# Optimization experiments

Hardware: AMD Instinct MI355X
Metric: run time of the kernel (lower is better)

The kernel has to match this reference:

```python
import jax, jax.numpy as jnp
import numpy as np

N_KNN = 20
BN_EPS = 1e-5
LRELU_SLOPE = 0.2


def setup_inputs() -> dict:
    key = jax.random.key(0)
    k1, k2, k3 = jax.random.split(key, 3)
    B, C, N = 4, 3, 8192
    x = jax.random.normal(k1, (B, C, N), dtype=jnp.float32)
    # Conv2d(1, 16, 1): weight [16,1,1,1] -> flatten to [16]; bias [16]
    conv_w = jax.random.normal(k2, (16,), dtype=jnp.float32) * (1.0 / np.sqrt(1.0))
    conv_b = jax.random.normal(k3, (16,), dtype=jnp.float32) * 0.01
    gamma = jnp.ones((16,), dtype=jnp.float32)
    beta = jnp.zeros((16,), dtype=jnp.float32)
    return {"x": x, "conv_w": conv_w, "conv_b": conv_b, "gamma": gamma, "beta": beta}


def reference(x, conv_w, conv_b, gamma, beta):
    # x: [B, C, N]
    pts = jnp.transpose(x, (0, 2, 1))  # [B, N, C]
    sq = jnp.sum(pts * pts, axis=-1)  # [B, N]
    # pairwise squared distances, clamped for numerical safety
    d2 = sq[:, :, None] + sq[:, None, :] - 2.0 * jnp.einsum("bnc,bmc->bnm", pts, pts)
    d2 = jnp.maximum(d2, 0.0)
    # safe sqrt: zero gradient at zero distance (matches torch.cdist behavior)
    dist = jnp.where(d2 > 0, jnp.sqrt(jnp.where(d2 > 0, d2, 1.0)), 0.0)  # [B, N, N]
    # k smallest distances = k largest of negated
    neg_topk, _ = jax.lax.top_k(-dist, N_KNN)
    knn = -neg_topk  # [B, N, K], ascending
    # 1x1 conv (1 -> 16 channels): feat[b,c,n,k] = w[c]*knn[b,n,k] + b[c]
    feat = knn[:, None, :, :] * conv_w[None, :, None, None] + conv_b[None, :, None, None]  # [B,16,N,K]
    # BatchNorm2d in training mode: per-channel stats over (B, N, K), biased variance
    mean = jnp.mean(feat, axis=(0, 2, 3), keepdims=True)
    var = jnp.mean((feat - mean) ** 2, axis=(0, 2, 3), keepdims=True)
    xhat = (feat - mean) * jax.lax.rsqrt(var + BN_EPS)
    y = gamma[None, :, None, None] * xhat + beta[None, :, None, None]
    # LeakyReLU(0.2)
    y = jnp.where(y >= 0, y, LRELU_SLOPE * y)
    # max over k neighbors
    return jnp.max(y, axis=-1)  # [B, 16, N]
```

## Files before the change

kernel.cpp:

```cpp
#include <hip/hip_runtime.h>
#include <stdint.h>

#define NPTS  8192
#define NB    4
#define KNN   20
#define NROWS (NB * NPTS)
#define MTOTF 655360.0f
#define WPB   8
#define BLK   (WPB * 64)
#define SLICE (NPTS / WPB)
#define LSTR  (KNN + 1)
#define CAP   12
#define NEG_INF -3.0e38f

__device__ __forceinline__ float med3f(float a, float b, float c) {
    return __builtin_amdgcn_fmed3f(a, b, c);
}

__device__ __forceinline__ unsigned enc_f(float f) {
    unsigned u = __float_as_uint(f);
    return (u & 0x80000000u) ? ~u : (u | 0x80000000u);
}
__device__ __forceinline__ float dec_f(unsigned u) {
    return __uint_as_float((u & 0x80000000u) ? (u & 0x7fffffffu) : ~u);
}

__device__ __forceinline__ void insert_t(float arr[KNN], float t) {
#pragma unroll
    for (int j = KNN - 1; j > 0; --j) arr[j] = med3f(t, arr[j - 1], arr[j]);
    arr[0] = fmaxf(arr[0], t);
}

__device__ __forceinline__ void flush_buf(float arr[KNN], int& cnt,
    const float* bufw, int lane, unsigned* threshS) {
#pragma unroll
    for (int s = 0; s < CAP; ++s) {
        const float v = bufw[s * 64 + lane];
        insert_t(arr, (s < cnt) ? v : NEG_INF);
    }
    cnt = 0;
    atomicMax(&threshS[lane], enc_f(arr[KNN - 1]));
}

__device__ __forceinline__ void finalize_row(
    float arr[KNN], float px, float py, float pz, int row, int lane,
    float* __restrict__ kmaxA, float* __restrict__ kminA, float* __restrict__ acc)
{
    const float pn2 = px * px + py * py + pz * pz;
    float sum = 0.f, sum2 = 0.f, dmin = 0.f, dmax = 0.f;
#pragma unroll
    for (int k = 0; k < KNN; ++k) {
        float d2 = fmaxf(fmaf(-2.f, arr[k], pn2), 0.f);
        float d = sqrtf(d2);
        sum += d; sum2 += d2;
        if (k == 0) dmin = d;
        dmax = d;
    }
    kmaxA[row] = dmax;
    kminA[row] = dmin;
#pragma unroll
    for (int o = 32; o; o >>= 1) {
        sum  += __shfl_down(sum,  o, 64);
        sum2 += __shfl_down(sum2, o, 64);
    }
    if (lane == 0) { atomicAdd(acc, sum); atomicAdd(acc + 1, sum2); }
}

__global__ __launch_bounds__(256) void prep_kernel(
    const float* __restrict__ x, float4* __restrict__ tile4, float* __restrict__ acc)
{
    const int i = blockIdx.x * 256 + threadIdx.x;
    const int b = i >> 13;
    const int m = i & (NPTS - 1);
    const float* xb = x + b * 3 * NPTS;
    const float qx = xb[m], qy = xb[NPTS + m], qz = xb[2 * NPTS + m];
    tile4[i] = make_float4(qx, qy, qz, -0.5f * (qx * qx + qy * qy + qz * qz));
    if (i < 2) acc[i] = 0.f;
}

__global__ __launch_bounds__(BLK, 8) void knn_kernel(
    const float* __restrict__ x, const float4* __restrict__ tile4,
    float* __restrict__ kmaxA, float* __restrict__ kminA, float* __restrict__ acc)
{
    __shared__ float shmem[(WPB - 1) * 64 * LSTR];
    __shared__ unsigned threshS[64];

    const int tid  = threadIdx.x;
    const int lane = tid & 63;
    const int wave = __builtin_amdgcn_readfirstlane(tid >> 6);
    const int rowBase = blockIdx.x * 64;
    const int row  = rowBase + lane;
    const int b    = rowBase >> 13;
    const int n    = row & (NPTS - 1);
    const float* xb = x + b * 3 * NPTS;

    const float px = xb[n];
    const float py = xb[NPTS + n];
    const float pz = xb[2 * NPTS + n];

    if (tid < 64) threshS[tid] = enc_f(NEG_INF);

    float arr[KNN];
#pragma unroll
    for (int j = 0; j < KNN; ++j) arr[j] = NEG_INF;

    float* bufw = shmem + wave * (CAP * 64);
    int cnt = 0;
    __syncthreads();

    const float4* __restrict__ tp = tile4 + b * NPTS + wave * SLICE;
    float th = NEG_INF;
    for (int c = 0; c < SLICE / 32; ++c) {
        th = dec_f(*(volatile unsigned*)(threshS + lane));
        const float4* tq = tp + c * 32;
        for (int g = 0; g < 8; ++g) {
#pragma unroll
            for (int u = 0; u < 4; ++u) {
                const float4 q = tq[g * 4 + u];
                const float t = fmaf(q.x, px, fmaf(q.y, py, fmaf(q.z, pz, q.w)));
                if (t > th) { bufw[cnt * 64 + lane] = t; ++cnt; }
            }
            if (__any(cnt > CAP - 4)) {
                flush_buf(arr, cnt, bufw, lane, threshS);
                th = dec_f(*(volatile unsigned*)(threshS + lane));
            }
        }
    }
    if (__any(cnt > 0)) flush_buf(arr, cnt, bufw, lane, threshS);
    __syncthreads();

    if (wave > 0) {
        float* dst = shmem + ((wave - 1) * 64 + lane) * LSTR;
#pragma unroll
        for (int j = 0; j < KNN; ++j) dst[j] = arr[j];
    }
    __syncthreads();

    if (wave == 0) {
        for (int wsrc = 0; wsrc < WPB - 1; ++wsrc) {
            const float* src = shmem + (wsrc * 64 + lane) * LSTR;
#pragma unroll
            for (int k = 0; k < KNN; ++k) insert_t(arr, src[k]);
        }
        finalize_row(arr, px, py, pz, row, lane, kmaxA, kminA, acc);
    }
}

__global__ __launch_bounds__(BLK) void knn_kernel_lds(
    const float* __restrict__ x,
    float* __restrict__ kmaxA, float* __restrict__ kminA, float* __restrict__ acc)
{
    __shared__ float4 tile[2048];
    __shared__ float  lists[(WPB - 1) * 64 * LSTR];

    const int tid  = threadIdx.x;
    const int lane = tid & 63;
    const int wave = tid >> 6;
    const int rowBase = blockIdx.x * 64;
    const int row  = rowBase + lane;
    const int b    = rowBase >> 13;
    const int n    = row & (NPTS - 1);
    const float* xb = x + b * 3 * NPTS;

    const float px = xb[n];
    const float py = xb[NPTS + n];
    const float pz = xb[2 * NPTS + n];

    float arr[KNN];
#pragma unroll
    for (int j = 0; j < KNN; ++j) arr[j] = NEG_INF;

    for (int t0 = 0; t0 < NPTS; t0 += 2048) {
        __syncthreads();
        const int i4 = tid * 4;
        const float4 qx4 = *(const float4*)(xb + t0 + i4);
        const float4 qy4 = *(const float4*)(xb + NPTS + t0 + i4);
        const float4 qz4 = *(const float4*)(xb + 2 * NPTS + t0 + i4);
        tile[i4 + 0] = make_float4(qx4.x, qy4.x, qz4.x, -0.5f * (qx4.x*qx4.x + qy4.x*qy4.x + qz4.x*qz4.x));
        tile[i4 + 1] = make_float4(qx4.y, qy4.y, qz4.y, -0.5f * (qx4.y*qx4.y + qy4.y*qy4.y + qz4.y*qz4.y));
        tile[i4 + 2] = make_float4(qx4.z, qy4.z, qz4.z, -0.5f * (qx4.z*qx4.z + qy4.z*qy4.z + qz4.z*qz4.z));
        tile[i4 + 3] = make_float4(qx4.w, qy4.w, qz4.w, -0.5f * (qx4.w*qx4.w + qy4.w*qy4.w + qz4.w*qz4.w));
        __syncthreads();
        const float4* base = tile + wave * 256;
#pragma unroll 4
        for (int i = 0; i < 256; ++i) {
            const float4 q = base[i];
            float t = fmaf(q.x, px, fmaf(q.y, py, fmaf(q.z, pz, q.w)));
            insert_t(arr, t);
        }
    }
    __syncthreads();

    if (wave > 0) {
        float* dst = lists + ((wave - 1) * 64 + lane) * LSTR;
#pragma unroll
        for (int j = 0; j < KNN; ++j) dst[j] = arr[j];
    }
    __syncthreads();

    if (wave == 0) {
        for (int wsrc = 0; wsrc < WPB - 1; ++wsrc) {
            const float* src = lists + (wsrc * 64 + lane) * LSTR;
#pragma unroll
            for (int k = 0; k < KNN; ++k) insert_t(arr, src[k]);
        }
        finalize_row(arr, px, py, pz, row, lane, kmaxA, kminA, acc);
    }
}

__global__ __launch_bounds__(256) void out_kernel(
    const float* __restrict__ kmaxA, const float* __restrict__ kminA,
    const float* __restrict__ acc,
    const float* __restrict__ w, const float* __restrict__ gamma,
    const float* __restrict__ beta, float* __restrict__ out)
{
    const int r = blockIdx.x * 256 + threadIdx.x;
    const int b = r >> 13;
    const int n = r & (NPTS - 1);
    const float mu  = acc[0] * (1.0f / MTOTF);
    float var = acc[1] * (1.0f / MTOTF) - mu * mu;
    var = fmaxf(var, 0.f);
    const float kmax = kmaxA[r];
    const float kmin = kminA[r];
#pragma unroll
    for (int c = 0; c < 16; ++c) {
        const float wc = w[c];
        const float a = gamma[c] * wc * rsqrtf(wc * wc * var + 1e-5f);
        const float d = beta[c] - a * mu;
        float v = a * (a >= 0.f ? kmax : kmin) + d;
        v = (v >= 0.f) ? v : 0.2f * v;
        out[(b * 16 + c) * NPTS + n] = v;
    }
}

extern "C" void kernel_launch(void* const* d_in, const int* in_sizes, int n_in,
                              void* d_out, int out_size, void* d_ws, size_t ws_size,
                              hipStream_t stream)
{
    const float* x     = (const float*)d_in[0];
    const float* w     = (const float*)d_in[1];
    const float* gamma = (const float*)d_in[3];
    const float* beta  = (const float*)d_in[4];
    float* out = (float*)d_out;
    float* ws  = (float*)d_ws;

    float* kmaxA = ws;
    float* kminA = ws + NROWS;
    float* acc   = ws + 2 * NROWS;
    float4* tile4 = (float4*)(ws + 2 * NROWS + 4);
    const size_t need = (size_t)(2 * NROWS + 4) * 4 + (size_t)NROWS * 16;

    if (ws_size >= need) {
        prep_kernel<<<NROWS / 256, 256, 0, stream>>>(x, tile4, acc);
        knn_kernel<<<NROWS / 64, BLK, 0, stream>>>(x, tile4, kmaxA, kminA, acc);
    } else {
        prep_kernel<<<1, 256, 0, stream>>>(x, tile4, acc);
        knn_kernel_lds<<<NROWS / 64, BLK, 0, stream>>>(x, kmaxA, kminA, acc);
    }
    out_kernel<<<NROWS / 256, 256, 0, stream>>>(kmaxA, kminA, acc, w, gamma, beta, out);
}
```

Measured before the change: 206.3 us.

## Split KNN candidate scan into two halves per row block and merge

The candidate scan now runs as two blocks per 64-row group, each covering half of the points, and writes partial top-20 lists to workspace. A new merge kernel combines the two lists and finalizes the statistics. The buffered flush is also made dynamic with a larger buffer that skips empty groups of four. The aim is more blocks in flight to fill the GPU, at the cost of an extra kernel launch, extra global traffic for the partial lists, and weaker pruning thresholds within each half.

```diff
diff --git a/kernel.cpp b/kernel.cpp
--- a/kernel.cpp
+++ b/kernel.cpp
@@ -9,8 +9,11 @@
 #define WPB   8
 #define BLK   (WPB * 64)
 #define SLICE (NPTS / WPB)
+#define HALF  (NPTS / 2)
+#define SLICE2 (HALF / WPB)
 #define LSTR  (KNN + 1)
 #define CAP   12
+#define CAP2  16
 #define NEG_INF -3.0e38f
 
 __device__ __forceinline__ float med3f(float a, float b, float c) {
@@ -37,6 +40,22 @@
     for (int s = 0; s < CAP; ++s) {
         const float v = bufw[s * 64 + lane];
         insert_t(arr, (s < cnt) ? v : NEG_INF);
+    }
+    cnt = 0;
+    atomicMax(&threshS[lane], enc_f(arr[KNN - 1]));
+}
+
+__device__ __forceinline__ void flush_dyn(float arr[KNN], int& cnt,
+    const float* bufw, int lane, unsigned* threshS) {
+#pragma unroll
+    for (int s0 = 0; s0 < CAP2; s0 += 4) {
+        if (__any(cnt > s0)) {
+#pragma unroll
+            for (int s = s0; s < s0 + 4; ++s) {
+                const float v = bufw[s * 64 + lane];
+                insert_t(arr, (s < cnt) ? v : NEG_INF);
+            }
+        }
     }
     cnt = 0;
     atomicMax(&threshS[lane], enc_f(arr[KNN - 1]));
@@ -76,6 +95,115 @@
     const float qx = xb[m], qy = xb[NPTS + m], qz = xb[2 * NPTS + m];
     tile4[i] = make_float4(qx, qy, qz, -0.5f * (qx * qx + qy * qy + qz * qz));
     if (i < 2) acc[i] = 0.f;
+}
+
+__global__ __launch_bounds__(BLK, 8) void knn_split_kernel(
+    const float* __restrict__ x, const float4* __restrict__ tile4,
+    float* __restrict__ part)
+{
+    __shared__ float shmem[(WPB - 1) * 64 * LSTR];
+    __shared__ unsigned threshS[64];
+
+    const int tid  = threadIdx.x;
+    const int lane = tid & 63;
+    const int wave = __builtin_amdgcn_readfirstlane(tid >> 6);
+    const int rb   = blockIdx.x >> 1;
+    const int half = blockIdx.x & 1;
+    const int rowBase = rb * 64;
+    const int row  = rowBase + lane;
+    const int b    = rowBase >> 13;
+    const int n    = row & (NPTS - 1);
+    const float* xb = x + b * 3 * NPTS;
+
+    const float px = xb[n];
+    const float py = xb[NPTS + n];
+    const float pz = xb[2 * NPTS + n];
+
+    if (tid < 64) threshS[tid] = enc_f(NEG_INF);
+
+    float arr[KNN];
+#pragma unroll
+    for (int j = 0; j < KNN; ++j) arr[j] = NEG_INF;
+
+    float* bufw = shmem + wave * (CAP2 * 64);
+    __syncthreads();
+
+    const float4* __restrict__ tp = tile4 + b * NPTS + half * HALF + wave * SLICE2;
+
+#pragma unroll 8
+    for (int i = 0; i < 32; ++i) {
+        const float4 q = tp[i];
+        insert_t(arr, fmaf(q.x, px, fmaf(q.y, py, fmaf(q.z, pz, q.w))));
+    }
+    atomicMax(&threshS[lane], enc_f(arr[KNN - 1]));
+
+    int cnt = 0;
+    for (int c = 1; c < SLICE2 / 32; ++c) {
+        float th = dec_f(*(volatile unsigned*)(threshS + lane));
+        const float4* tq = tp + c * 32;
+        for (int g = 0; g < 8; ++g) {
+#pragma unroll
+            for (int u = 0; u < 4; ++u) {
+                const float4 q = tq[g * 4 + u];
+                const float t = fmaf(q.x, px, fmaf(q.y, py, fmaf(q.z, pz, q.w)));
+                bufw[cnt * 64 + lane] = t;
+                cnt += (t > th);
+            }
+            if (__any(cnt > CAP2 - 4)) {
+                flush_dyn(arr, cnt, bufw, lane, threshS);
+                th = dec_f(*(volatile unsigned*)(threshS + lane));
+            }
+        }
+    }
+    if (__any(cnt > 0)) flush_dyn(arr, cnt, bufw, lane, threshS);
+    __syncthreads();
+
+    if (wave > 0) {
+        float* dst = shmem + ((wave - 1) * 64 + lane) * LSTR;
+#pragma unroll
+        for (int j = 0; j < KNN; ++j) dst[j] = arr[j];
+    }
+    __syncthreads();
+
+    if (wave == 0) {
+        for (int wsrc = 0; wsrc < WPB - 1; ++wsrc) {
+            const float* src = shmem + (wsrc * 64 + lane) * LSTR;
+#pragma unroll
+            for (int k = 0; k < KNN; ++k) insert_t(arr, src[k]);
+        }
+        float4* dst = (float4*)(part + (row * 2 + half) * KNN);
+#pragma unroll
+        for (int k = 0; k < KNN; k += 4)
+            dst[k >> 2] = make_float4(arr[k], arr[k + 1], arr[k + 2], arr[k + 3]);
+    }
+}
+
+__global__ __launch_bounds__(256) void merge_kernel(
+    const float* __restrict__ x, const float* __restrict__ part,
+    float* __restrict__ kmaxA, float* __restrict__ kminA, float* __restrict__ acc)
+{
+    const int r = blockIdx.x * 256 + threadIdx.x;
+    const int lane = threadIdx.x & 63;
+    const int b = r >> 13;
+    const int n = r & (NPTS - 1);
+    const float* xb = x + b * 3 * NPTS;
+    const float px = xb[n];
+    const float py = xb[NPTS + n];
+    const float pz = xb[2 * NPTS + n];
+
+    const float4* pA = (const float4*)(part + r * 2 * KNN);
+    float arr[KNN];
+#pragma unroll
+    for (int k = 0; k < KNN; k += 4) {
+        const float4 v = pA[k >> 2];
+        arr[k] = v.x; arr[k + 1] = v.y; arr[k + 2] = v.z; arr[k + 3] = v.w;
+    }
+#pragma unroll
+    for (int k = 0; k < KNN; k += 4) {
+        const float4 v = pA[(KNN + k) >> 2];
+        insert_t(arr, v.x); insert_t(arr, v.y); insert_t(arr, v.z); insert_t(arr, v.w);
+    }
+    finalize_row(arr, px, py, pz, r, lane, kmaxA, kminA, acc);
 }
 
 __global__ __launch_bounds__(BLK, 8) void knn_kernel(
@@ -248,9 +376,15 @@
     float* kminA = ws + NROWS;
     float* acc   = ws + 2 * NROWS;
     float4* tile4 = (float4*)(ws + 2 * NROWS + 4);
-    const size_t need = (size_t)(2 * NROWS + 4) * 4 + (size_t)NROWS * 16;
-
-    if (ws_size >= need) {
+    float* part = ws + (2 * NROWS + 4) + 4 * NROWS;
+    const size_t need_tile  = (size_t)(2 * NROWS + 4) * 4 + (size_t)NROWS * 16;
+    const size_t need_split = need_tile + (size_t)NROWS * 2 * KNN * 4;
+
+    if (ws_size >= need_split) {
+        prep_kernel<<<NROWS / 256, 256, 0, stream>>>(x, tile4, acc);
+        knn_split_kernel<<<2 * (NROWS / 64), BLK, 0, stream>>>(x, tile4, part);
+        merge_kernel<<<NROWS / 256, 256, 0, stream>>>(x, part, kmaxA, kminA, acc);
+    } else if (ws_size >= need_tile) {
         prep_kernel<<<NROWS / 256, 256, 0, stream>>>(x, tile4, acc);
         knn_kernel<<<NROWS / 64, BLK, 0, stream>>>(x, tile4, kmaxA, kminA, acc);
     } else {
```

Result: no change. 202.5 us (-1.8%).
